# Kernel tuning notes

Hardware: AMD Instinct MI355X
Metric: run time of the kernel (lower is better)

Reference implementation:

```python
import jax, jax.numpy as jnp
import numpy as np

E_PROP = 0.8
DT = 0.02
AX = 0.2   # dt / tau_x = 0.02 / 0.1
AW = 0.02  # dt / tau_w = 0.02 / 1.0


def _ei_mask(out_size, in_size, e_prop, zero_prop, remove_diag):
    """EILinear mask: +1 for excitatory cols, -1 inhibitory, 0 for zeroed cols/diag."""
    e = int(e_prop * in_size)
    sign = np.ones(in_size, np.float32)
    sign[e:] = -1.0
    zc = int(round(zero_prop * in_size))
    exist = np.ones(in_size, np.float32)
    if zc > 0:
        exist[in_size - zc:] = 0.0
    m = np.tile((sign * exist)[None, :], (out_size, 1))
    if remove_diag:
        assert out_size == in_size
        m[np.eye(out_size, dtype=bool)] = 0.0
    return jnp.asarray(m)


def setup_inputs() -> dict:
    T, B, I, H, O = 32, 16, 128, 384, 32
    key = jax.random.key(0)
    ks = jax.random.split(key, 10)
    u = lambda k, s, hi: jax.random.uniform(k, s, jnp.float32, 0.0, hi)
    s_in = (1.0 / I) ** 0.5
    s_h = (1.0 / H) ** 0.5
    s_hz = (1.0 / (H - round((1.0 - E_PROP) * H))) ** 0.5  # zero_cols removed from fan-in
    return {
        "x": jax.random.normal(ks[0], (T, B, I), jnp.float32),
        "Rs": jax.random.uniform(ks[1], (T, B, 1), jnp.float32),
        "W_x2c": u(ks[2], (H, I), 0.5 * s_in),
        "W_c2c": u(ks[3], (H, H), s_h),
        "b_c2c": jnp.zeros((H,), jnp.float32),
        "W_c2h": u(ks[4], (H, H), 0.5 * s_hz),
        "W_h2h": u(ks[5], (H, H), s_h),
        "b_h2h": jnp.zeros((H,), jnp.float32),
        "W_h2o": u(ks[6], (O, H), 0.5 * s_hz),
        "W_attn": u(ks[7], (H, H), 0.1 * s_hz),
        "b_attn": jnp.zeros((H,), jnp.float32),
        "kappa": jnp.full((12,), AW, jnp.float32),
    }


def reference(x, Rs, W_x2c, W_c2c, b_c2c, W_c2h, W_h2h, b_h2h, W_h2o, W_attn, b_attn, kappa):
    T, B, I = x.shape
    H = W_c2c.shape[0]
    O = W_h2o.shape[0]
    retanh = lambda z: jnp.tanh(jax.nn.relu(z))

    m_x2c = _ei_mask(H, I, 1.0, 0.0, False)
    m_c2c = _ei_mask(H, H, E_PROP, 0.0, True)
    m_c2h = _ei_mask(H, H, 1.0, 1.0 - E_PROP, False)
    m_h2h = _ei_mask(H, H, E_PROP, 0.0, True)
    m_h2o = _ei_mask(O, H, 1.0, 1.0 - E_PROP, False)
    m_attn = _ei_mask(H, H, E_PROP, 1.0 - E_PROP, False)

    def plin(W, mask, w_fast, inp, bias=None):
        # (relu(W) + w_fast) * mask, per-batch matmul: [B,O,I] @ [B,I] -> [B,O]
        eff = (jax.nn.relu(W)[None] + w_fast) * mask[None]
        out = jnp.einsum('boi,bi->bo', eff, inp)
        return out if bias is None else out + bias

    def lin(W, mask, inp, bias=None):
        out = inp @ (jax.nn.relu(W) * mask).T
        return out if bias is None else out + bias

    def plast(w, R, pre, post, k, W_slow):
        # w: [B,O,I]; R: [B,1,1]; pre: [B,I]; post: [B,O]
        new_w = (w * (1.0 - AW)
                 + DT * R * (k[0] * pre[:, None, :]
                             + k[1] * post[:, :, None]
                             + k[2] * post[:, :, None] * pre[:, None, :]))
        lb = -jax.lax.stop_gradient(jax.nn.relu(W_slow))[None]
        return jnp.maximum(new_w, lb)

    def step(carry, inputs):
        x_t, R_t = inputs  # [B,I], [B,1]
        sc, oc, sh, oh, wxc, wcc, wch, whh = carry
        attn = retanh(lin(W_attn, m_attn, oh, b_attn))  # attention_type == 'bias'
        tic = plin(W_x2c, m_x2c, wxc, x_t) + plin(W_c2c, m_c2c, wcc, oc, b_c2c) + attn
        nsc = sc * (1.0 - AX) + tic * AX
        noc = retanh(nsc)
        tih = plin(W_c2h, m_c2h, wch, noc) + plin(W_h2h, m_h2h, whh, oh, b_h2h)
        nsh = sh * (1.0 - AX) + tih * AX
        noh = retanh(nsh)
        R = R_t[:, :, None]  # [B,1,1]
        wxc2 = plast(wxc, R, x_t, noc, kappa[0:3], W_x2c)
        wcc2 = plast(wcc, R, oc, noc, kappa[3:6], W_c2c)
        wch2 = plast(wch, R, noc, noh, kappa[6:9], W_c2h)
        whh2 = plast(whh, R, oh, noh, kappa[9:12], W_h2h)
        out_t = lin(W_h2o, m_h2o, noh)
        return (nsc, noc, nsh, noh, wxc2, wcc2, wch2, whh2), out_t

    z = jnp.zeros((B, H), x.dtype)
    carry0 = (z, z, z, z,
              jnp.zeros((B, H, I), x.dtype),
              jnp.zeros((B, H, H), x.dtype),
              jnp.zeros((B, H, H), x.dtype),
              jnp.zeros((B, H, H), x.dtype))
    _, outs = jax.lax.scan(step, carry0, (x, Rs))
    return outs  # [T, B, O]
```

## Files before the change

kernel.cpp:

```cpp
#include <hip/hip_runtime.h>


#define NT 32
#define NBATCH 16
#define DI 128
#define DH 384
#define DOUT 32
#define CSZ (NT * NBATCH * DH)

__device__ __forceinline__ float retanh_f(float z) {
  z = fmaxf(z, 0.0f);
  float e = __expf(-2.0f * z);
  return (1.0f - e) / (1.0f + e);
}

__device__ __forceinline__ float aldf(const float* p) {
  return __hip_atomic_load(p, __ATOMIC_RELAXED, __HIP_MEMORY_SCOPE_AGENT);
}
__device__ __forceinline__ void pubG(float* p, float v) {
  __hip_atomic_store(p, v, __ATOMIC_RELAXED, __HIP_MEMORY_SCOPE_AGENT);
}

__device__ __forceinline__ void gather6G(const float* src, int lane, float arr[6]) {
  const float* p = src + lane;
  float v0, v1, v2, v3, v4, v5;
  for (;;) {
    v0 = aldf(p + 0 * 64);
    v1 = aldf(p + 1 * 64);
    v2 = aldf(p + 2 * 64);
    v3 = aldf(p + 3 * 64);
    v4 = aldf(p + 4 * 64);
    v5 = aldf(p + 5 * 64);
    const bool ok = (v0 != 0.f) & (v1 != 0.f) & (v2 != 0.f) &
                    (v3 != 0.f) & (v4 != 0.f) & (v5 != 0.f);
    if (ok) break;
  }
  arr[0] = v0 - 2.f; arr[1] = v1 - 2.f; arr[2] = v2 - 2.f;
  arr[3] = v3 - 2.f; arr[4] = v4 - 2.f; arr[5] = v5 - 2.f;
}

__global__ __launch_bounds__(512, 2) void hrnn(
    const float* __restrict__ x, const float* __restrict__ Rs,
    const float* __restrict__ Wx, const float* __restrict__ Wc, const float* __restrict__ bc,
    const float* __restrict__ Wch, const float* __restrict__ Whh, const float* __restrict__ bh,
    const float* __restrict__ Wo, const float* __restrict__ Wa, const float* __restrict__ ba,
    const float* __restrict__ kap, float* __restrict__ out, float* __restrict__ comm) {
  const int tid  = threadIdx.x;
  const int lane = tid & 63;
  const int wv   = tid >> 6;
  const int bid  = blockIdx.x;
  const int b = ((bid & 7) << 1) | ((bid >> 3) & 1);
  const int k = bid >> 4;

  float* noc_buf = comm;
  float* noh_buf = comm + CSZ;

  __shared__ float sh_noh[DH];
  __shared__ float sh_noc[DH];

  const int og0 = k * 24 + wv * 3;
  const bool do_out = (k == 15);

  float wxc[3][2], wcc[3][6], wchv[3][5], whh[3][6];
  float rWx[3][2], rWc[3][6], rWch[3][5], rWhh[3][6], rWa[3][5];
  float sc[3], shs[3], bcr[3], bar[3], bhr[3];
  float ohr[6], ocr[6];
  float rWo[4][5];

#pragma unroll
  for (int r = 0; r < 3; ++r) {
    const int og = og0 + r;
#pragma unroll
    for (int j = 0; j < 2; ++j) { rWx[r][j] = fmaxf(Wx[og*DI + j*64 + lane], 0.f); wxc[r][j] = 0.f; }
#pragma unroll
    for (int j = 0; j < 6; ++j) { rWc[r][j] = fmaxf(Wc[og*DH + j*64 + lane], 0.f); wcc[r][j] = 0.f; }
#pragma unroll
    for (int j = 0; j < 5; ++j) { rWch[r][j] = fmaxf(Wch[og*DH + j*64 + lane], 0.f); wchv[r][j] = 0.f; }
#pragma unroll
    for (int j = 0; j < 6; ++j) { rWhh[r][j] = fmaxf(Whh[og*DH + j*64 + lane], 0.f); whh[r][j] = 0.f; }
#pragma unroll
    for (int j = 0; j < 5; ++j) {
      float w = fmaxf(Wa[og*DH + j*64 + lane], 0.f);
      rWa[r][j] = (j == 4 && lane >= 51) ? 0.f : w;
    }
    sc[r] = 0.f; shs[r] = 0.f;
    bcr[r] = bc[og]; bar[r] = ba[og]; bhr[r] = bh[og];
  }
  if (do_out) {
#pragma unroll
    for (int m = 0; m < 4; ++m) {
      const int o = wv * 4 + m;
#pragma unroll
      for (int j = 0; j < 5; ++j) {
        float w = fmaxf(Wo[o*DH + j*64 + lane], 0.f);
        rWo[m][j] = (j == 4 && lane >= 51) ? 0.f : w;
      }
    }
  }
#pragma unroll
  for (int j = 0; j < 6; ++j) { ohr[j] = 0.f; ocr[j] = 0.f; }
  float kp[12];
#pragma unroll
  for (int j = 0; j < 12; ++j) kp[j] = kap[j];

  float xp0 = x[b*DI + lane];
  float xp1 = x[b*DI + 64 + lane];
  float dtRp = 0.02f * Rs[b];

  for (int t = 0; t < NT; ++t) {
    const int toff = t * NBATCH * DH + b * DH;

    if (t > 0) {
      if (wv == 0) {
        float tmp[6];
        gather6G(noh_buf + toff - NBATCH * DH, lane, tmp);
#pragma unroll
        for (int j = 0; j < 6; ++j) sh_noh[j * 64 + lane] = tmp[j];
      }
      __syncthreads();
#pragma unroll
      for (int j = 0; j < 6; ++j) ohr[j] = sh_noh[j * 64 + lane];
    }

    const float dtR = dtRp;
    const float x0 = xp0;
    const float x1 = xp1;
    const float oh4s = (lane < 51) ? ohr[4] : -ohr[4];
    const float oc4s = (lane < 51) ? ocr[4] : -ocr[4];
    const float inC[6] = { ocr[0], ocr[1], ocr[2], ocr[3], oc4s, -ocr[5] };

    float nocr[3];
#pragma unroll
    for (int r = 0; r < 3; ++r) {
      const int og = og0 + r;
      const int dj = og >> 6, dl = og & 63;
      float accA = 0.f, accT = 0.f;
#pragma unroll
      for (int j = 0; j < 5; ++j) accA += rWa[r][j] * ohr[j];
      accT += (rWx[r][0] + wxc[r][0]) * x0;
      accT += (rWx[r][1] + wxc[r][1]) * x1;
#pragma unroll
      for (int j = 0; j < 6; ++j) {
        float term = (rWc[r][j] + wcc[r][j]) * inC[j];
        if (j == dj) term = (lane == dl) ? 0.f : term;
        accT += term;
      }
#pragma unroll
      for (int mm = 1; mm <= 32; mm <<= 1) {
        accA += __shfl_xor(accA, mm, 64);
        accT += __shfl_xor(accT, mm, 64);
      }
      const float attn = retanh_f(accA + bar[r]);
      const float tic = accT + bcr[r] + attn;
      sc[r] = 0.8f*sc[r] + 0.2f*tic;
      nocr[r] = retanh_f(sc[r]);
    }
    {
      float mine = (lane == 0) ? nocr[0] : (lane == 1) ? nocr[1] : nocr[2];
      if (lane < 3) pubG(noc_buf + toff + og0 + lane, mine + 2.0f);
    }

    if (t < NT-1) {
      xp0 = x[((t+1)*NBATCH + b)*DI + lane];
      xp1 = x[((t+1)*NBATCH + b)*DI + 64 + lane];
      dtRp = 0.02f * Rs[(t+1)*NBATCH + b];
    }
    if (do_out && t > 0) {
#pragma unroll
      for (int m = 0; m < 4; ++m) {
        float a = 0.f;
#pragma unroll
        for (int j = 0; j < 5; ++j) a += rWo[m][j] * ohr[j];
#pragma unroll
        for (int mm = 1; mm <= 32; mm <<= 1) a += __shfl_xor(a, mm, 64);
        if (lane == 0) out[(t-1)*NBATCH*DOUT + b*DOUT + wv*4 + m] = a;
      }
    }
    if (t < NT-1) {
      float axc[2], bxc[2];
#pragma unroll
      for (int j = 0; j < 2; ++j) {
        const float pre = (j == 0) ? x0 : x1;
        axc[j] = dtR*kp[0]*pre; bxc[j] = dtR*(kp[1] + kp[2]*pre);
      }
      float acc_[6], bcc_[6];
#pragma unroll
      for (int j = 0; j < 6; ++j) { acc_[j] = dtR*kp[3]*ocr[j]; bcc_[j] = dtR*(kp[4] + kp[5]*ocr[j]); }
#pragma unroll
      for (int r = 0; r < 3; ++r) {
        const float post = nocr[r];
#pragma unroll
        for (int j = 0; j < 2; ++j)
          wxc[r][j] = fmaxf(fmaf(wxc[r][j], 0.98f, fmaf(bxc[j], post, axc[j])), -rWx[r][j]);
#pragma unroll
        for (int j = 0; j < 6; ++j)
          wcc[r][j] = fmaxf(fmaf(wcc[r][j], 0.98f, fmaf(bcc_[j], post, acc_[j])), -rWc[r][j]);
      }
    }

    if (wv == 0) {
      float tmp[6];
      gather6G(noc_buf + toff, lane, tmp);
#pragma unroll
      for (int j = 0; j < 6; ++j) sh_noc[j * 64 + lane] = tmp[j];
    }
    __syncthreads();
    float ncr[6];
#pragma unroll
    for (int j = 0; j < 6; ++j) ncr[j] = sh_noc[j * 64 + lane];

    const float nc4z = (lane < 51) ? ncr[4] : 0.f;
    const float inH[6] = { ohr[0], ohr[1], ohr[2], ohr[3], oh4s, -ohr[5] };
    const float inN[5] = { ncr[0], ncr[1], ncr[2], ncr[3], nc4z };
    float nohr[3];
#pragma unroll
    for (int r = 0; r < 3; ++r) {
      const int og = og0 + r;
      const int dj = og >> 6, dl = og & 63;
      float acc = 0.f;
#pragma unroll
      for (int j = 0; j < 5; ++j) acc += (rWch[r][j] + wchv[r][j]) * inN[j];
#pragma unroll
      for (int j = 0; j < 6; ++j) {
        float term = (rWhh[r][j] + whh[r][j]) * inH[j];
        if (j == dj) term = (lane == dl) ? 0.f : term;
        acc += term;
      }
#pragma unroll
      for (int mm = 1; mm <= 32; mm <<= 1) acc += __shfl_xor(acc, mm, 64);
      const float tih = acc + bhr[r];
      shs[r] = 0.8f*shs[r] + 0.2f*tih;
      nohr[r] = retanh_f(shs[r]);
    }
    {
      float mine = (lane == 0) ? nohr[0] : (lane == 1) ? nohr[1] : nohr[2];
      if (lane < 3) pubG(noh_buf + toff + og0 + lane, mine + 2.0f);
    }

    if (t < NT-1) {
      float an_[5], bn_[5];
#pragma unroll
      for (int j = 0; j < 5; ++j) { an_[j] = dtR*kp[6]*ncr[j]; bn_[j] = dtR*(kp[7] + kp[8]*ncr[j]); }
      float ah_[6], bh_[6];
#pragma unroll
      for (int j = 0; j < 6; ++j) { ah_[j] = dtR*kp[9]*ohr[j]; bh_[j] = dtR*(kp[10] + kp[11]*ohr[j]); }
#pragma unroll
      for (int r = 0; r < 3; ++r) {
        const float post = nohr[r];
#pragma unroll
        for (int j = 0; j < 5; ++j)
          wchv[r][j] = fmaxf(fmaf(wchv[r][j], 0.98f, fmaf(bn_[j], post, an_[j])), -rWch[r][j]);
#pragma unroll
        for (int j = 0; j < 6; ++j)
          whh[r][j] = fmaxf(fmaf(whh[r][j], 0.98f, fmaf(bh_[j], post, ah_[j])), -rWhh[r][j]);
      }
    }
#pragma unroll
    for (int j = 0; j < 6; ++j) ocr[j] = ncr[j];
  }

  if (do_out) {
    if (wv == 0) {
      float tmp[6];
      gather6G(noh_buf + (NT-1)*NBATCH*DH + b*DH, lane, tmp);
#pragma unroll
      for (int j = 0; j < 6; ++j) sh_noh[j * 64 + lane] = tmp[j];
    }
    __syncthreads();
    float oh2[6];
#pragma unroll
    for (int j = 0; j < 6; ++j) oh2[j] = sh_noh[j * 64 + lane];
#pragma unroll
    for (int m = 0; m < 4; ++m) {
      float a = 0.f;
#pragma unroll
      for (int j = 0; j < 5; ++j) a += rWo[m][j] * oh2[j];
#pragma unroll
      for (int mm = 1; mm <= 32; mm <<= 1) a += __shfl_xor(a, mm, 64);
      if (lane == 0) out[(NT-1)*NBATCH*DOUT + b*DOUT + wv*4 + m] = a;
    }
  }
}

extern "C" void kernel_launch(void* const* d_in, const int* in_sizes, int n_in,
                              void* d_out, int out_size, void* d_ws, size_t ws_size,
                              hipStream_t stream) {
  const float* x   = (const float*)d_in[0];
  const float* Rs  = (const float*)d_in[1];
  const float* Wx  = (const float*)d_in[2];
  const float* Wc  = (const float*)d_in[3];
  const float* bc  = (const float*)d_in[4];
  const float* Wch = (const float*)d_in[5];
  const float* Whh = (const float*)d_in[6];
  const float* bh  = (const float*)d_in[7];
  const float* Wo  = (const float*)d_in[8];
  const float* Wa  = (const float*)d_in[9];
  const float* ba  = (const float*)d_in[10];
  const float* kap = (const float*)d_in[11];
  float* out = (float*)d_out;

  float* comm = (float*)d_ws;
  hipMemsetAsync(comm, 0, (size_t)2 * CSZ * sizeof(float), stream);

  hipLaunchKernelGGL(hrnn, dim3(256), dim3(512), 0, stream,
                     x, Rs, Wx, Wc, bc, Wch, Whh, bh, Wo, Wa, ba, kap,
                     out, comm);
}
```

Measured before the change: 170.0 us.

## Split cortical and hidden layer updates into separate block roles

The grid doubles to 512 blocks. Half of them compute the c-layer (x2c, c2c, attention, readout) and the other half compute the h-layer (c2h, h2h), and they exchange states through global flag-encoded buffers. Each role holds only its own weights and plastic state in registers, so launch_bounds now asks for 4 blocks per SM. A combined 12-value gather waits on both the noc and noh buffers in one spin loop. The intent is to pipeline the two layers across blocks and cut register pressure. The cost is more cross-block spinning, and the scheme depends on all 512 blocks being co-resident.

```diff
diff --git a/kernel.cpp b/kernel.cpp
--- a/kernel.cpp
+++ b/kernel.cpp
@@ -25,12 +25,8 @@
   const float* p = src + lane;
   float v0, v1, v2, v3, v4, v5;
   for (;;) {
-    v0 = aldf(p + 0 * 64);
-    v1 = aldf(p + 1 * 64);
-    v2 = aldf(p + 2 * 64);
-    v3 = aldf(p + 3 * 64);
-    v4 = aldf(p + 4 * 64);
-    v5 = aldf(p + 5 * 64);
+    v0 = aldf(p + 0 * 64); v1 = aldf(p + 1 * 64); v2 = aldf(p + 2 * 64);
+    v3 = aldf(p + 3 * 64); v4 = aldf(p + 4 * 64); v5 = aldf(p + 5 * 64);
     const bool ok = (v0 != 0.f) & (v1 != 0.f) & (v2 != 0.f) &
                     (v3 != 0.f) & (v4 != 0.f) & (v5 != 0.f);
     if (ok) break;
@@ -39,7 +35,29 @@
   arr[3] = v3 - 2.f; arr[4] = v4 - 2.f; arr[5] = v5 - 2.f;
 }
 
-__global__ __launch_bounds__(512, 2) void hrnn(
+__device__ __forceinline__ void gather12G(const float* srcA, const float* srcB,
+                                          int lane, float arrA[6], float arrB[6]) {
+  const float* pa = srcA + lane;
+  const float* pb = srcB + lane;
+  float a0,a1,a2,a3,a4,a5,b0,b1,b2,b3,b4,b5;
+  for (;;) {
+    a0 = aldf(pa + 0*64); a1 = aldf(pa + 1*64); a2 = aldf(pa + 2*64);
+    a3 = aldf(pa + 3*64); a4 = aldf(pa + 4*64); a5 = aldf(pa + 5*64);
+    b0 = aldf(pb + 0*64); b1 = aldf(pb + 1*64); b2 = aldf(pb + 2*64);
+    b3 = aldf(pb + 3*64); b4 = aldf(pb + 4*64); b5 = aldf(pb + 5*64);
+    const bool ok = (a0 != 0.f) & (a1 != 0.f) & (a2 != 0.f) &
+                    (a3 != 0.f) & (a4 != 0.f) & (a5 != 0.f) &
+                    (b0 != 0.f) & (b1 != 0.f) & (b2 != 0.f) &
+                    (b3 != 0.f) & (b4 != 0.f) & (b5 != 0.f);
+    if (ok) break;
+  }
+  arrA[0] = a0 - 2.f; arrA[1] = a1 - 2.f; arrA[2] = a2 - 2.f;
+  arrA[3] = a3 - 2.f; arrA[4] = a4 - 2.f; arrA[5] = a5 - 2.f;
+  arrB[0] = b0 - 2.f; arrB[1] = b1 - 2.f; arrB[2] = b2 - 2.f;
+  arrB[3] = b3 - 2.f; arrB[4] = b4 - 2.f; arrB[5] = b5 - 2.f;
+}
+
+__global__ __launch_bounds__(512, 4) void hrnn(
     const float* __restrict__ x, const float* __restrict__ Rs,
     const float* __restrict__ Wx, const float* __restrict__ Wc, const float* __restrict__ bc,
     const float* __restrict__ Wch, const float* __restrict__ Whh, const float* __restrict__ bh,
@@ -49,235 +67,255 @@
   const int lane = tid & 63;
   const int wv   = tid >> 6;
   const int bid  = blockIdx.x;
-  const int b = ((bid & 7) << 1) | ((bid >> 3) & 1);
-  const int k = bid >> 4;
+  const bool roleA = (bid < 256);
+  const int sub = bid & 255;
+  const int b = ((sub & 7) << 1) | ((sub >> 3) & 1);
+  const int k = sub >> 4;
+  const int og0 = k * 24 + wv * 3;
 
   float* noc_buf = comm;
   float* noh_buf = comm + CSZ;
 
+  __shared__ float sh_noc[DH];
   __shared__ float sh_noh[DH];
-  __shared__ float sh_noc[DH];
-
-  const int og0 = k * 24 + wv * 3;
-  const bool do_out = (k == 15);
-
-  float wxc[3][2], wcc[3][6], wchv[3][5], whh[3][6];
-  float rWx[3][2], rWc[3][6], rWch[3][5], rWhh[3][6], rWa[3][5];
-  float sc[3], shs[3], bcr[3], bar[3], bhr[3];
-  float ohr[6], ocr[6];
-  float rWo[4][5];
-
-#pragma unroll
-  for (int r = 0; r < 3; ++r) {
-    const int og = og0 + r;
-#pragma unroll
-    for (int j = 0; j < 2; ++j) { rWx[r][j] = fmaxf(Wx[og*DI + j*64 + lane], 0.f); wxc[r][j] = 0.f; }
-#pragma unroll
-    for (int j = 0; j < 6; ++j) { rWc[r][j] = fmaxf(Wc[og*DH + j*64 + lane], 0.f); wcc[r][j] = 0.f; }
-#pragma unroll
-    for (int j = 0; j < 5; ++j) { rWch[r][j] = fmaxf(Wch[og*DH + j*64 + lane], 0.f); wchv[r][j] = 0.f; }
-#pragma unroll
-    for (int j = 0; j < 6; ++j) { rWhh[r][j] = fmaxf(Whh[og*DH + j*64 + lane], 0.f); whh[r][j] = 0.f; }
-#pragma unroll
-    for (int j = 0; j < 5; ++j) {
-      float w = fmaxf(Wa[og*DH + j*64 + lane], 0.f);
-      rWa[r][j] = (j == 4 && lane >= 51) ? 0.f : w;
-    }
-    sc[r] = 0.f; shs[r] = 0.f;
-    bcr[r] = bc[og]; bar[r] = ba[og]; bhr[r] = bh[og];
-  }
-  if (do_out) {
-#pragma unroll
-    for (int m = 0; m < 4; ++m) {
-      const int o = wv * 4 + m;
+
+  if (roleA) {
+    float wxc[3][2], wcc[3][6], rWx[3][2], rWc[3][6], rWa[3][5];
+    float sc[3], bcr[3], bar3[3], kpA[6];
+    float rWo[4][5];
+    const bool do_out = (k == 15);
+    float ohr[6], ocr[6];
+
+#pragma unroll
+    for (int r = 0; r < 3; ++r) {
+      const int og = og0 + r;
+#pragma unroll
+      for (int j = 0; j < 2; ++j) { rWx[r][j] = fmaxf(Wx[og*DI + j*64 + lane], 0.f); wxc[r][j] = 0.f; }
+#pragma unroll
+      for (int j = 0; j < 6; ++j) { rWc[r][j] = fmaxf(Wc[og*DH + j*64 + lane], 0.f); wcc[r][j] = 0.f; }
 #pragma unroll
       for (int j = 0; j < 5; ++j) {
-        float w = fmaxf(Wo[o*DH + j*64 + lane], 0.f);
-        rWo[m][j] = (j == 4 && lane >= 51) ? 0.f : w;
-      }
-    }
-  }
-#pragma unroll
-  for (int j = 0; j < 6; ++j) { ohr[j] = 0.f; ocr[j] = 0.f; }
-  float kp[12];
-#pragma unroll
-  for (int j = 0; j < 12; ++j) kp[j] = kap[j];
-
-  float xp0 = x[b*DI + lane];
-  float xp1 = x[b*DI + 64 + lane];
-  float dtRp = 0.02f * Rs[b];
-
-  for (int t = 0; t < NT; ++t) {
-    const int toff = t * NBATCH * DH + b * DH;
-
-    if (t > 0) {
+        float w = fmaxf(Wa[og*DH + j*64 + lane], 0.f);
+        rWa[r][j] = (j == 4 && lane >= 51) ? 0.f : w;
+      }
+      sc[r] = 0.f; bcr[r] = bc[og]; bar3[r] = ba[og];
+    }
+#pragma unroll
+    for (int j = 0; j < 6; ++j) kpA[j] = kap[j];
+    if (do_out) {
+#pragma unroll
+      for (int m = 0; m < 4; ++m) {
+        const int o = wv * 4 + m;
+#pragma unroll
+        for (int j = 0; j < 5; ++j) {
+          float w = fmaxf(Wo[o*DH + j*64 + lane], 0.f);
+          rWo[m][j] = (j == 4 && lane >= 51) ? 0.f : w;
+        }
+      }
+    }
+#pragma unroll
+    for (int j = 0; j < 6; ++j) { ohr[j] = 0.f; ocr[j] = 0.f; }
+    float xp0 = x[b*DI + lane];
+    float xp1 = x[b*DI + 64 + lane];
+    float dtRp = 0.02f * Rs[b];
+
+    for (int t = 0; t < NT; ++t) {
+      const int toff = t * NBATCH * DH + b * DH;
+      if (t > 0) {
+        const int poff = toff - NBATCH * DH;
+        if (wv == 0) {
+          float ta[6], tb[6];
+          gather12G(noc_buf + poff, noh_buf + poff, lane, ta, tb);
+#pragma unroll
+          for (int j = 0; j < 6; ++j) { sh_noc[j*64 + lane] = ta[j]; sh_noh[j*64 + lane] = tb[j]; }
+        }
+        __syncthreads();
+#pragma unroll
+        for (int j = 0; j < 6; ++j) { ocr[j] = sh_noc[j*64 + lane]; ohr[j] = sh_noh[j*64 + lane]; }
+      }
+      const float x0 = xp0, x1 = xp1, dtR = dtRp;
+      const float oc4s = (lane < 51) ? ocr[4] : -ocr[4];
+      const float inC[6] = { ocr[0], ocr[1], ocr[2], ocr[3], oc4s, -ocr[5] };
+      float nocr[3];
+#pragma unroll
+      for (int r = 0; r < 3; ++r) {
+        const int og = og0 + r;
+        const int dj = og >> 6, dl = og & 63;
+        float accA = 0.f, accT = 0.f;
+#pragma unroll
+        for (int j = 0; j < 5; ++j) accA += rWa[r][j] * ohr[j];
+        accT += (rWx[r][0] + wxc[r][0]) * x0;
+        accT += (rWx[r][1] + wxc[r][1]) * x1;
+#pragma unroll
+        for (int j = 0; j < 6; ++j) {
+          float term = (rWc[r][j] + wcc[r][j]) * inC[j];
+          if (j == dj) term = (lane == dl) ? 0.f : term;
+          accT += term;
+        }
+#pragma unroll
+        for (int mm = 1; mm <= 32; mm <<= 1) {
+          accA += __shfl_xor(accA, mm, 64);
+          accT += __shfl_xor(accT, mm, 64);
+        }
+        const float attn = retanh_f(accA + bar3[r]);
+        const float tic = accT + bcr[r] + attn;
+        sc[r] = 0.8f*sc[r] + 0.2f*tic;
+        nocr[r] = retanh_f(sc[r]);
+      }
+      {
+        float mine = (lane == 0) ? nocr[0] : (lane == 1) ? nocr[1] : nocr[2];
+        if (lane < 3) pubG(noc_buf + toff + og0 + lane, mine + 2.0f);
+      }
+      if (do_out && t > 0) {
+#pragma unroll
+        for (int m = 0; m < 4; ++m) {
+          float a = 0.f;
+#pragma unroll
+          for (int j = 0; j < 5; ++j) a += rWo[m][j] * ohr[j];
+#pragma unroll
+          for (int mm = 1; mm <= 32; mm <<= 1) a += __shfl_xor(a, mm, 64);
+          if (lane == 0) out[(t-1)*NBATCH*DOUT + b*DOUT + wv*4 + m] = a;
+        }
+      }
+      if (t < NT-1) {
+        float axc[2], bxc[2];
+#pragma unroll
+        for (int j = 0; j < 2; ++j) {
+          const float pre = (j == 0) ? x0 : x1;
+          axc[j] = dtR*kpA[0]*pre; bxc[j] = dtR*(kpA[1] + kpA[2]*pre);
+        }
+        float acc_[6], bcc_[6];
+#pragma unroll
+        for (int j = 0; j < 6; ++j) { acc_[j] = dtR*kpA[3]*ocr[j]; bcc_[j] = dtR*(kpA[4] + kpA[5]*ocr[j]); }
+#pragma unroll
+        for (int r = 0; r < 3; ++r) {
+          const float post = nocr[r];
+#pragma unroll
+          for (int j = 0; j < 2; ++j)
+            wxc[r][j] = fmaxf(fmaf(wxc[r][j], 0.98f, fmaf(bxc[j], post, axc[j])), -rWx[r][j]);
+#pragma unroll
+          for (int j = 0; j < 6; ++j)
+            wcc[r][j] = fmaxf(fmaf(wcc[r][j], 0.98f, fmaf(bcc_[j], post, acc_[j])), -rWc[r][j]);
+        }
+        xp0 = x[((t+1)*NBATCH + b)*DI + lane];
+        xp1 = x[((t+1)*NBATCH + b)*DI + 64 + lane];
+        dtRp = 0.02f * Rs[(t+1)*NBATCH + b];
+      }
+    }
+    if (do_out) {
       if (wv == 0) {
         float tmp[6];
-        gather6G(noh_buf + toff - NBATCH * DH, lane, tmp);
-#pragma unroll
-        for (int j = 0; j < 6; ++j) sh_noh[j * 64 + lane] = tmp[j];
+        gather6G(noh_buf + (NT-1)*NBATCH*DH + b*DH, lane, tmp);
+#pragma unroll
+        for (int j = 0; j < 6; ++j) sh_noh[j*64 + lane] = tmp[j];
       }
       __syncthreads();
-#pragma unroll
-      for (int j = 0; j < 6; ++j) ohr[j] = sh_noh[j * 64 + lane];
-    }
-
-    const float dtR = dtRp;
-    const float x0 = xp0;
-    const float x1 = xp1;
-    const float oh4s = (lane < 51) ? ohr[4] : -ohr[4];
-    const float oc4s = (lane < 51) ? ocr[4] : -ocr[4];
-    const float inC[6] = { ocr[0], ocr[1], ocr[2], ocr[3], oc4s, -ocr[5] };
-
-    float nocr[3];
+      float oh2[6];
+#pragma unroll
+      for (int j = 0; j < 6; ++j) oh2[j] = sh_noh[j*64 + lane];
+#pragma unroll
+      for (int m = 0; m < 4; ++m) {
+        float a = 0.f;
+#pragma unroll
+        for (int j = 0; j < 5; ++j) a += rWo[m][j] * oh2[j];
+#pragma unroll
+        for (int mm = 1; mm <= 32; mm <<= 1) a += __shfl_xor(a, mm, 64);
+        if (lane == 0) out[(NT-1)*NBATCH*DOUT + b*DOUT + wv*4 + m] = a;
+      }
+    }
+  } else {
+    float wchv[3][5], whh[3][6], rWch[3][5], rWhh[3][6];
+    float shs[3], bhr[3], kpB[6];
+    float ohr[6];
+
 #pragma unroll
     for (int r = 0; r < 3; ++r) {
       const int og = og0 + r;
-      const int dj = og >> 6, dl = og & 63;
-      float accA = 0.f, accT = 0.f;
-#pragma unroll
-      for (int j = 0; j < 5; ++j) accA += rWa[r][j] * ohr[j];
-      accT += (rWx[r][0] + wxc[r][0]) * x0;
-      accT += (rWx[r][1] + wxc[r][1]) * x1;
-#pragma unroll
-      for (int j = 0; j < 6; ++j) {
-        float term = (rWc[r][j] + wcc[r][j]) * inC[j];
-        if (j == dj) term = (lane == dl) ? 0.f : term;
-        accT += term;
-      }
-#pragma unroll
-      for (int mm = 1; mm <= 32; mm <<= 1) {
-        accA += __shfl_xor(accA, mm, 64);
-        accT += __shfl_xor(accT, mm, 64);
-      }
-      const float attn = retanh_f(accA + bar[r]);
-      const float tic = accT + bcr[r] + attn;
-      sc[r] = 0.8f*sc[r] + 0.2f*tic;
-      nocr[r] = retanh_f(sc[r]);
-    }
-    {
-      float mine = (lane == 0) ? nocr[0] : (lane == 1) ? nocr[1] : nocr[2];
-      if (lane < 3) pubG(noc_buf + toff + og0 + lane, mine + 2.0f);
-    }
-
-    if (t < NT-1) {
-      xp0 = x[((t+1)*NBATCH + b)*DI + lane];
-      xp1 = x[((t+1)*NBATCH + b)*DI + 64 + lane];
-      dtRp = 0.02f * Rs[(t+1)*NBATCH + b];
-    }
-    if (do_out && t > 0) {
-#pragma unroll
-      for (int m = 0; m < 4; ++m) {
-        float a = 0.f;
-#pragma unroll
-        for (int j = 0; j < 5; ++j) a += rWo[m][j] * ohr[j];
-#pragma unroll
-        for (int mm = 1; mm <= 32; mm <<= 1) a += __shfl_xor(a, mm, 64);
-        if (lane == 0) out[(t-1)*NBATCH*DOUT + b*DOUT + wv*4 + m] = a;
-      }
-    }
-    if (t < NT-1) {
-      float axc[2], bxc[2];
-#pragma unroll
-      for (int j = 0; j < 2; ++j) {
-        const float pre = (j == 0) ? x0 : x1;
-        axc[j] = dtR*kp[0]*pre; bxc[j] = dtR*(kp[1] + kp[2]*pre);
-      }
-      float acc_[6], bcc_[6];
-#pragma unroll
-      for (int j = 0; j < 6; ++j) { acc_[j] = dtR*kp[3]*ocr[j]; bcc_[j] = dtR*(kp[4] + kp[5]*ocr[j]); }
+#pragma unroll
+      for (int j = 0; j < 5; ++j) { rWch[r][j] = fmaxf(Wch[og*DH + j*64 + lane], 0.f); wchv[r][j] = 0.f; }
+#pragma unroll
+      for (int j = 0; j < 6; ++j) { rWhh[r][j] = fmaxf(Whh[og*DH + j*64 + lane], 0.f); whh[r][j] = 0.f; }
+      shs[r] = 0.f; bhr[r] = bh[og];
+    }
+#pragma unroll
+    for (int j = 0; j < 6; ++j) kpB[j] = kap[6 + j];
+#pragma unroll
+    for (int j = 0; j < 6; ++j) ohr[j] = 0.f;
+    float dtRp = 0.02f * Rs[b];
+
+    for (int t = 0; t < NT; ++t) {
+      const int toff = t * NBATCH * DH + b * DH;
+      if (wv == 0) {
+        if (t == 0) {
+          float ta[6];
+          gather6G(noc_buf + toff, lane, ta);
+#pragma unroll
+          for (int j = 0; j < 6; ++j) sh_noc[j*64 + lane] = ta[j];
+        } else {
+          float ta[6], tb[6];
+          gather12G(noc_buf + toff, noh_buf + toff - NBATCH*DH, lane, ta, tb);
+#pragma unroll
+          for (int j = 0; j < 6; ++j) { sh_noc[j*64 + lane] = ta[j]; sh_noh[j*64 + lane] = tb[j]; }
+        }
+      }
+      __syncthreads();
+      float ncr[6];
+#pragma unroll
+      for (int j = 0; j < 6; ++j) ncr[j] = sh_noc[j*64 + lane];
+      if (t > 0) {
+#pragma unroll
+        for (int j = 0; j < 6; ++j) ohr[j] = sh_noh[j*64 + lane];
+      }
+      const float dtR = dtRp;
+      const float nc4z = (lane < 51) ? ncr[4] : 0.f;
+      const float oh4s = (lane < 51) ? ohr[4] : -ohr[4];
+      const float inH[6] = { ohr[0], ohr[1], ohr[2], ohr[3], oh4s, -ohr[5] };
+      const float inN[5] = { ncr[0], ncr[1], ncr[2], ncr[3], nc4z };
+      float nohr[3];
 #pragma unroll
       for (int r = 0; r < 3; ++r) {
-        const float post = nocr[r];
-#pragma unroll
-        for (int j = 0; j < 2; ++j)
-          wxc[r][j] = fmaxf(fmaf(wxc[r][j], 0.98f, fmaf(bxc[j], post, axc[j])), -rWx[r][j]);
-#pragma unroll
-        for (int j = 0; j < 6; ++j)
-          wcc[r][j] = fmaxf(fmaf(wcc[r][j], 0.98f, fmaf(bcc_[j], post, acc_[j])), -rWc[r][j]);
-      }
-    }
-
-    if (wv == 0) {
-      float tmp[6];
-      gather6G(noc_buf + toff, lane, tmp);
-#pragma unroll
-      for (int j = 0; j < 6; ++j) sh_noc[j * 64 + lane] = tmp[j];
-    }
-    __syncthreads();
-    float ncr[6];
-#pragma unroll
-    for (int j = 0; j < 6; ++j) ncr[j] = sh_noc[j * 64 + lane];
-
-    const float nc4z = (lane < 51) ? ncr[4] : 0.f;
-    const float inH[6] = { ohr[0], ohr[1], ohr[2], ohr[3], oh4s, -ohr[5] };
-    const float inN[5] = { ncr[0], ncr[1], ncr[2], ncr[3], nc4z };
-    float nohr[3];
-#pragma unroll
-    for (int r = 0; r < 3; ++r) {
-      const int og = og0 + r;
-      const int dj = og >> 6, dl = og & 63;
-      float acc = 0.f;
-#pragma unroll
-      for (int j = 0; j < 5; ++j) acc += (rWch[r][j] + wchv[r][j]) * inN[j];
-#pragma unroll
-      for (int j = 0; j < 6; ++j) {
-        float term = (rWhh[r][j] + whh[r][j]) * inH[j];
-        if (j == dj) term = (lane == dl) ? 0.f : term;
-        acc += term;
-      }
-#pragma unroll
-      for (int mm = 1; mm <= 32; mm <<= 1) acc += __shfl_xor(acc, mm, 64);
-      const float tih = acc + bhr[r];
-      shs[r] = 0.8f*shs[r] + 0.2f*tih;
-      nohr[r] = retanh_f(shs[r]);
-    }
-    {
-      float mine = (lane == 0) ? nohr[0] : (lane == 1) ? nohr[1] : nohr[2];
-      if (lane < 3) pubG(noh_buf + toff + og0 + lane, mine + 2.0f);
-    }
-
-    if (t < NT-1) {
-      float an_[5], bn_[5];
-#pragma unroll
-      for (int j = 0; j < 5; ++j) { an_[j] = dtR*kp[6]*ncr[j]; bn_[j] = dtR*(kp[7] + kp[8]*ncr[j]); }
-      float ah_[6], bh_[6];
-#pragma unroll
-      for (int j = 0; j < 6; ++j) { ah_[j] = dtR*kp[9]*ohr[j]; bh_[j] = dtR*(kp[10] + kp[11]*ohr[j]); }
-#pragma unroll
-      for (int r = 0; r < 3; ++r) {
-        const float post = nohr[r];
-#pragma unroll
-        for (int j = 0; j < 5; ++j)
-          wchv[r][j] = fmaxf(fmaf(wchv[r][j], 0.98f, fmaf(bn_[j], post, an_[j])), -rWch[r][j]);
-#pragma unroll
-        for (int j = 0; j < 6; ++j)
-          whh[r][j] = fmaxf(fmaf(whh[r][j], 0.98f, fmaf(bh_[j], post, ah_[j])), -rWhh[r][j]);
-      }
-    }
-#pragma unroll
-    for (int j = 0; j < 6; ++j) ocr[j] = ncr[j];
-  }
-
-  if (do_out) {
-    if (wv == 0) {
-      float tmp[6];
-      gather6G(noh_buf + (NT-1)*NBATCH*DH + b*DH, lane, tmp);
-#pragma unroll
-      for (int j = 0; j < 6; ++j) sh_noh[j * 64 + lane] = tmp[j];
-    }
-    __syncthreads();
-    float oh2[6];
-#pragma unroll
-    for (int j = 0; j < 6; ++j) oh2[j] = sh_noh[j * 64 + lane];
-#pragma unroll
-    for (int m = 0; m < 4; ++m) {
-      float a = 0.f;
-#pragma unroll
-      for (int j = 0; j < 5; ++j) a += rWo[m][j] * oh2[j];
-#pragma unroll
-      for (int mm = 1; mm <= 32; mm <<= 1) a += __shfl_xor(a, mm, 64);
-      if (lane == 0) out[(NT-1)*NBATCH*DOUT + b*DOUT + wv*4 + m] = a;
+        const int og = og0 + r;
+        const int dj = og >> 6, dl = og & 63;
+        float acc = 0.f;
+#pragma unroll
+        for (int j = 0; j < 5; ++j) acc += (rWch[r][j] + wchv[r][j]) * inN[j];
+#pragma unroll
+        for (int j = 0; j < 6; ++j) {
+          float term = (rWhh[r][j] + whh[r][j]) * inH[j];
+          if (j == dj) term = (lane == dl) ? 0.f : term;
+          acc += term;
+        }
+#pragma unroll
+        for (int mm = 1; mm <= 32; mm <<= 1) acc += __shfl_xor(acc, mm, 64);
+        const float tih = acc + bhr[r];
+        shs[r] = 0.8f*shs[r] + 0.2f*tih;
+        nohr[r] = retanh_f(shs[r]);
+      }
+      {
+        float mine = (lane == 0) ? nohr[0] : (lane == 1) ? nohr[1] : nohr[2];
+        if (lane < 3) pubG(noh_buf + toff + og0 + lane, mine + 2.0f);
+      }
+      if (t < NT-1) {
+        float an_[5], bn_[5];
+#pragma unroll
+        for (int j = 0; j < 5; ++j) { an_[j] = dtR*kpB[0]*ncr[j]; bn_[j] = dtR*(kpB[1] + kpB[2]*ncr[j]); }
+        float ah_[6], bh_[6];
+#pragma unroll
+        for (int j = 0; j < 6; ++j) { ah_[j] = dtR*kpB[3]*ohr[j]; bh_[j] = dtR*(kpB[4] + kpB[5]*ohr[j]); }
+#pragma unroll
+        for (int r = 0; r < 3; ++r) {
+          const float post = nohr[r];
+#pragma unroll
+          for (int j = 0; j < 5; ++j)
+            wchv[r][j] = fmaxf(fmaf(wchv[r][j], 0.98f, fmaf(bn_[j], post, an_[j])), -rWch[r][j]);
+#pragma unroll
+          for (int j = 0; j < 6; ++j)
+            whh[r][j] = fmaxf(fmaf(whh[r][j], 0.98f, fmaf(bh_[j], post, ah_[j])), -rWhh[r][j]);
+        }
+        dtRp = 0.02f * Rs[(t+1)*NBATCH + b];
+      }
+#pragma unroll
+      for (int j = 0; j < 6; ++j) ohr[j] = (j < 6) ? ohr[j] : ohr[j];
     }
   }
 }
@@ -302,7 +340,7 @@
   float* comm = (float*)d_ws;
   hipMemsetAsync(comm, 0, (size_t)2 * CSZ * sizeof(float), stream);
 
-  hipLaunchKernelGGL(hrnn, dim3(256), dim3(512), 0, stream,
+  hipLaunchKernelGGL(hrnn, dim3(512), dim3(512), 0, stream,
                      x, Rs, Wx, Wc, bc, Wch, Whh, bh, Wo, Wa, ba, kap,
                      out, comm);
 }
```

Result: slower. 265.6 us (+56.2%).
